# Performance work log

Measured on AMD Instinct MI355X. Metric: run time of the kernel, lower is better.

Reference implementation:

```python
import jax, jax.numpy as jnp
import numpy as np
import math

B, C, H, W = 8, 64, 256, 256
E, NH = 256, 8
HD = E // NH  # 32


def get_coords(h, w):
    xx, yy = jnp.meshgrid(jnp.arange(h, dtype=jnp.float32), jnp.arange(w, dtype=jnp.float32), indexing='ij')
    return jnp.stack((xx.reshape(-1), yy.reshape(-1)), axis=-1)  # [N, 2]


def setup_inputs() -> dict:
    key = jax.random.key(0)
    ks = jax.random.split(key, 12)
    def xavier(k, shape):
        fan_out, fan_in = shape
        a = math.sqrt(6.0 / (fan_in + fan_out))
        return jax.random.uniform(k, shape, jnp.float32, -a, a)
    x = jax.random.normal(ks[0], (B, C, H, W), jnp.float32)
    z = jax.random.normal(ks[1], (B, C), jnp.float32)
    pos = jax.random.uniform(ks[2], (B, NH, 2), jnp.float32) * (H - 1)
    Wq = xavier(ks[3], (E, C)); bq = jnp.zeros((E,), jnp.float32)
    Wk = xavier(ks[4], (E, C)); bk = jnp.zeros((E,), jnp.float32)
    Wv = xavier(ks[5], (E, C)); bv = jnp.zeros((E,), jnp.float32)
    Wp = xavier(ks[6], (HD, 2)); bp = jax.random.uniform(ks[7], (HD,), jnp.float32, -1.0, 1.0) / math.sqrt(2.0)
    return {"x": x, "z": z, "pos": pos, "Wq": Wq, "bq": bq, "Wk": Wk, "bk": bk,
            "Wv": Wv, "bv": bv, "Wp": Wp, "bp": bp}


def reference(x, z, pos, Wq, bq, Wk, bk, Wv, bv, Wp, bp):
    b, c, h, w = x.shape
    n = h * w
    x_flat = x.reshape(b, c, n).transpose(0, 2, 1)          # [B, N, C]
    pos_grid = get_coords(h, w)                              # [N, 2]
    q = (z @ Wq.T + bq).reshape(b, NH, HD)                   # [B, H, hd]
    k = (x_flat @ Wk.T + bk).reshape(b, n, NH, HD)           # [B, N, H, hd]
    # relative-position modulation of keys
    rel = pos_grid[None, :, None, :] - pos[:, None, :, :]    # [B, N, H, 2]
    qxk = rel @ Wp.T + bp                                    # [B, N, H, hd]
    k = k * qxk
    v = x_flat @ Wv.T + bv                                   # [B, N, E]
    attn_logits = jnp.einsum('bhc,bnhc->bnh', q, k) / math.sqrt(HD)
    attention = jax.nn.softmax(attn_logits, axis=1)          # softmax over N
    pos_out = jnp.einsum('bnh,nx->bhx', attention, pos_grid) # [B, H, 2]
    values = jnp.einsum('bnh,bnc->bhc', attention, v)        # [B, H, E]
    return (values, pos_out)
```

## Files before the change

### kernel.cpp

```cpp
#include <hip/hip_runtime.h>

#define NN    65536
#define NSUB  256
#define NBLK  (NN/NSUB)

typedef short bf16x8 __attribute__((ext_vector_type(8)));
typedef float f32x4v __attribute__((ext_vector_type(4)));
typedef unsigned short ushort_t;
typedef unsigned int uint_t;

#define XSTR   72
#define XHI_B  0
#define XLO_B  36864
#define LGA_B  36864
#define LGSTR  28
#define RED_B  73728
#define SMEM_BYTES 74240

#define WTHI_B  0
#define WTLO_B  32768
#define CJ_B    65536
#define PM_B    66304
#define PL_B    131840
#define PSP_B   197376
#define PSX_B   328448
#define Q_B     4522752
#define QSTR    68

__device__ __forceinline__ uint_t bf16_rne_bits(float f) {
  uint_t u = __float_as_uint(f);
  return (u + 0x7FFFu + ((u >> 16) & 1u)) >> 16;
}
template <int CTRL>
__device__ __forceinline__ float dpp_add(float x) {
  int t = __builtin_amdgcn_update_dpp(0, __float_as_int(x), CTRL, 0xf, 0xf, false);
  return x + __int_as_float(t);
}
template <int CTRL>
__device__ __forceinline__ float dpp_maxs(float x) {
  int t = __builtin_amdgcn_update_dpp((int)0xFF800000u, __float_as_int(x), CTRL, 0xf, 0xf, false);
  return fmaxf(x, __int_as_float(t));
}
__device__ __forceinline__ float wave_sum(float x) {
  x = dpp_add<0x111>(x); x = dpp_add<0x112>(x); x = dpp_add<0x114>(x);
  x = dpp_add<0x118>(x); x = dpp_add<0x142>(x); x = dpp_add<0x143>(x);
  return __int_as_float(__builtin_amdgcn_readlane(__float_as_int(x), 63));
}
__device__ __forceinline__ float wave_max(float x) {
  x = dpp_maxs<0x111>(x); x = dpp_maxs<0x112>(x); x = dpp_maxs<0x114>(x);
  x = dpp_maxs<0x118>(x); x = dpp_maxs<0x142>(x); x = dpp_maxs<0x143>(x);
  return __int_as_float(__builtin_amdgcn_readlane(__float_as_int(x), 63));
}

__global__ __launch_bounds__(64) void prep_kernel(
    const float* __restrict__ z,  const float* __restrict__ Wq, const float* __restrict__ bq,
    const float* __restrict__ Wk, const float* __restrict__ bk,
    const float* __restrict__ Wp, const float* __restrict__ bp,
    ushort_t* __restrict__ WThi, ushort_t* __restrict__ WTlo, float* __restrict__ Cj)
{
  const int h = blockIdx.x, b = blockIdx.y, t = threadIdx.x;
  __shared__ float q[32];
  if (t < 32) {
    const int e = h*32 + t;
    float a = bq[e];
    const float* zr = z + b*64;
    const float* wr = Wq + e*64;
    #pragma unroll 8
    for (int c = 0; c < 64; ++c) a += zr[c]*wr[c];
    q[t] = a;
  }
  __syncthreads();
  const int c = t;
  float w[3] = {0.f, 0.f, 0.f};
  #pragma unroll 4
  for (int hd = 0; hd < 32; ++hd) {
    const float qk = q[hd] * Wk[(h*32+hd)*64 + c];
    w[0] += qk * bp[hd];
    w[1] += qk * Wp[hd*2+0];
    w[2] += qk * Wp[hd*2+1];
  }
  #pragma unroll
  for (int j = 0; j < 3; ++j) {
    const int coeff = h*3 + j;
    const uint_t hb = bf16_rne_bits(w[j]);
    const float  fh = __uint_as_float(hb << 16);
    const uint_t lb = bf16_rne_bits(w[j] - fh);
    WThi[(b*32 + coeff)*64 + c] = (ushort_t)hb;
    WTlo[(b*32 + coeff)*64 + c] = (ushort_t)lb;
  }
  if (h == 0) {
    #pragma unroll
    for (int r = 0; r < 8; ++r) {
      WThi[(b*32 + 24 + r)*64 + c] = 0;
      WTlo[(b*32 + 24 + r)*64 + c] = 0;
    }
  }
  if (t < 3) {
    float s = 0.f;
    for (int hd = 0; hd < 32; ++hd) {
      const float m = (t == 0) ? bp[hd] : Wp[hd*2 + (t-1)];
      s += q[hd] * m * bk[h*32+hd];
    }
    Cj[b*24 + h*3 + t] = s;
  }
}

__global__ __launch_bounds__(256, 2) void main_kernel(
    const float* __restrict__ x, const float* __restrict__ pos,
    const ushort_t* __restrict__ WThi, const ushort_t* __restrict__ WTlo,
    const float* __restrict__ Cj,
    float* __restrict__ Pm, float* __restrict__ Pl,
    float* __restrict__ Psp, float* __restrict__ Psx)
{
  extern __shared__ char smc[];
  ushort_t* xhi = (ushort_t*)(smc + XHI_B);
  ushort_t* xlo = (ushort_t*)(smc + XLO_B);
  float*    lga = (float*)(smc + LGA_B);
  float*    red = (float*)(smc + RED_B);
  const int t   = threadIdx.x;
  const int blk = blockIdx.x;
  const int b   = blockIdx.y;
  const int n0  = blk * NSUB;
  const int wid = t >> 6, lid = t & 63;
  const int c0  = lid & 15, q4 = lid >> 4;

  bf16x8 bh[2][2], bl[2][2];
  {
    const ushort_t* wtb_h = WThi + b*2048;
    const ushort_t* wtb_l = WTlo + b*2048;
    #pragma unroll
    for (int nt = 0; nt < 2; ++nt)
      #pragma unroll
      for (int ks = 0; ks < 2; ++ks) {
        const int off = (nt*16 + c0)*64 + ks*32 + q4*8;
        bh[nt][ks] = *(const bf16x8*)(wtb_h + off);
        bl[nt][ks] = *(const bf16x8*)(wtb_l + off);
      }
  }

  {
    const float* xg = x + (size_t)b*64*NN + n0 + t;
    #pragma unroll
    for (int cc = 0; cc < 4; ++cc) {
      float v[16];
      #pragma unroll
      for (int i = 0; i < 16; ++i) v[i] = xg[(size_t)(cc*16+i)*NN];
      uint_t hb[16], lb[16];
      #pragma unroll
      for (int i = 0; i < 16; ++i) {
        hb[i] = bf16_rne_bits(v[i]);
        lb[i] = bf16_rne_bits(v[i] - __uint_as_float(hb[i] << 16));
      }
      uint4 H0 = make_uint4(hb[0]|(hb[1]<<16), hb[2]|(hb[3]<<16), hb[4]|(hb[5]<<16), hb[6]|(hb[7]<<16));
      uint4 H1 = make_uint4(hb[8]|(hb[9]<<16), hb[10]|(hb[11]<<16), hb[12]|(hb[13]<<16), hb[14]|(hb[15]<<16));
      uint4 L0 = make_uint4(lb[0]|(lb[1]<<16), lb[2]|(lb[3]<<16), lb[4]|(lb[5]<<16), lb[6]|(lb[7]<<16));
      uint4 L1 = make_uint4(lb[8]|(lb[9]<<16), lb[10]|(lb[11]<<16), lb[12]|(lb[13]<<16), lb[14]|(lb[15]<<16));
      char* dh = smc + XHI_B + t*144 + cc*32;
      char* dl = smc + XLO_B + t*144 + cc*32;
      *(uint4*)(dh)      = H0;  *(uint4*)(dh + 16) = H1;
      *(uint4*)(dl)      = L0;  *(uint4*)(dl + 16) = L1;
    }
  }

  float cj[24];
  {
    const float* cjp = Cj + b*24;
    #pragma unroll
    for (int k = 0; k < 24; ++k) cj[k] = cjp[k];
  }
  float rxh[8], py[8];
  #pragma unroll
  for (int h = 0; h < 8; ++h) {
    rxh[h] = (float)blk - pos[(b*8+h)*2 + 0];
    py[h]  = pos[(b*8+h)*2 + 1];
  }

  __syncthreads();

  f32x4v acc[4][2];
  #pragma unroll
  for (int mt = 0; mt < 4; ++mt) { acc[mt][0] = (f32x4v)0.f; acc[mt][1] = (f32x4v)0.f; }
  {
    const int mrow0 = wid*64;
    #pragma unroll
    for (int mt = 0; mt < 4; ++mt) {
      const int row = mrow0 + mt*16 + c0;
      const ushort_t* ph = xhi + row*XSTR + q4*8;
      const ushort_t* pl = xlo + row*XSTR + q4*8;
      bf16x8 ah0 = *(const bf16x8*)(ph);
      bf16x8 ah1 = *(const bf16x8*)(ph + 32);
      bf16x8 al0 = *(const bf16x8*)(pl);
      bf16x8 al1 = *(const bf16x8*)(pl + 32);
      #pragma unroll
      for (int nt = 0; nt < 2; ++nt) {
        f32x4v a = acc[mt][nt];
        a = __builtin_amdgcn_mfma_f32_16x16x32_bf16(ah0, bh[nt][0], a, 0, 0, 0);
        a = __builtin_amdgcn_mfma_f32_16x16x32_bf16(ah1, bh[nt][1], a, 0, 0, 0);
        a = __builtin_amdgcn_mfma_f32_16x16x32_bf16(ah0, bl[nt][0], a, 0, 0, 0);
        a = __builtin_amdgcn_mfma_f32_16x16x32_bf16(ah1, bl[nt][1], a, 0, 0, 0);
        a = __builtin_amdgcn_mfma_f32_16x16x32_bf16(al0, bh[nt][0], a, 0, 0, 0);
        a = __builtin_amdgcn_mfma_f32_16x16x32_bf16(al1, bh[nt][1], a, 0, 0, 0);
        acc[mt][nt] = a;
      }
    }
  }
  __syncthreads();

  {
    const int mrow0 = wid*64;
    #pragma unroll
    for (int mt = 0; mt < 4; ++mt)
      #pragma unroll
      for (int r = 0; r < 4; ++r) {
        const int prow = mrow0 + mt*16 + q4*4 + r;
        lga[prow*LGSTR + c0] = acc[mt][0][r];
        if (c0 < 8) lga[prow*LGSTR + 16 + c0] = acc[mt][1][r];
      }
  }
  __syncthreads();

  float a24[24];
  {
    const float4* ap = (const float4*)(lga + t*LGSTR);
    #pragma unroll
    for (int r = 0; r < 6; ++r) *(float4*)(a24 + 4*r) = ap[r];
  }
  const float tf = (float)t;
  float lg[8];
  #pragma unroll
  for (int h = 0; h < 8; ++h) {
    const float a0 = a24[h*3+0] + cj[h*3+0];
    const float a1 = a24[h*3+1] + cj[h*3+1];
    const float a2 = a24[h*3+2] + cj[h*3+2];
    lg[h] = (a0 + rxh[h]*a1 + (tf - py[h])*a2) * 0.17677669529663687f;
  }

  #pragma unroll
  for (int h = 0; h < 8; ++h) {
    const float m = wave_max(lg[h]);
    if (lid == 0) red[h*4 + wid] = m;
  }
  __syncthreads();

  float p[8];
  #pragma unroll
  for (int h = 0; h < 8; ++h) {
    const float M = fmaxf(fmaxf(red[h*4+0], red[h*4+1]), fmaxf(red[h*4+2], red[h*4+3]));
    p[h] = __expf(lg[h] - M);
  }
  #pragma unroll
  for (int h = 0; h < 8; ++h) {
    const float sp  = wave_sum(p[h]);
    const float spj = wave_sum(p[h] * tf);
    if (lid == 0) { red[32 + h*4 + wid] = sp; red[64 + h*4 + wid] = spj; }
  }
  __syncthreads();

  if (t < 8) {
    const int base = (b*NBLK + blk)*8 + t;
    const float M = fmaxf(fmaxf(red[t*4+0], red[t*4+1]), fmaxf(red[t*4+2], red[t*4+3]));
    const float L  = red[32+t*4+0] + red[32+t*4+1] + red[32+t*4+2] + red[32+t*4+3];
    const float SJ = red[64+t*4+0] + red[64+t*4+1] + red[64+t*4+2] + red[64+t*4+3];
    Pm[base] = M;
    Pl[base] = L;
    Psp[base*2+0] = (float)blk * L;
    Psp[base*2+1] = SJ;
  }

  float aB[8];
  #pragma unroll
  for (int h = 0; h < 8; ++h) aB[h] = 0.f;
  {
    const ushort_t* xrow = xhi + (wid*64)*XSTR + lid;
    #pragma unroll 8
    for (int j = 0; j < 64; ++j) {
      const float xv = __uint_as_float(((uint_t)xrow[j*XSTR]) << 16);
      #pragma unroll
      for (int h = 0; h < 8; ++h) {
        const float pj = __int_as_float(__builtin_amdgcn_readlane(__float_as_int(p[h]), j));
        aB[h] = fmaf(pj, xv, aB[h]);
      }
    }
  }
  __syncthreads();
  {
    float* pstage = (float*)smc;
    #pragma unroll
    for (int h = 0; h < 8; ++h) pstage[(wid*8 + h)*64 + lid] = aB[h];
  }
  __syncthreads();
  {
    const float* pstage = (const float*)smc;
    const size_t pb = ((size_t)(b*NBLK + blk))*8;
    #pragma unroll
    for (int r = 0; r < 2; ++r) {
      const int idx = t + 256*r;
      const float s = pstage[idx] + pstage[512+idx] + pstage[1024+idx] + pstage[1536+idx];
      Psx[pb*64 + idx] = s;
    }
  }
}

__global__ __launch_bounds__(256) void reduce1_kernel(
    const float* __restrict__ Pm, const float* __restrict__ Pl,
    const float* __restrict__ Psp, const float* __restrict__ Psx,
    float* __restrict__ Q)
{
  const int g = blockIdx.x, h = blockIdx.y, b = blockIdx.z, t = threadIdx.x;
  __shared__ float al[32];
  __shared__ float mgs;
  __shared__ float sums[3];
  __shared__ float sxl[256];
  const int base = (b*NBLK + g*32)*8 + h;

  float m_t = -1e30f;
  if (t < 32) m_t = Pm[base + t*8];
  if (t < 64) {
    float mm = m_t;
    #pragma unroll
    for (int off = 16; off >= 1; off >>= 1) mm = fmaxf(mm, __shfl_xor(mm, off, 64));
    if (t == 0) mgs = mm;
  }
  __syncthreads();
  const float Mg = mgs;
  if (t < 32) {
    const float a = __expf(m_t - Mg);
    al[t] = a;
    float lt = Pl[base + t*8] * a;
    float sx = Psp[(base + t*8)*2 + 0] * a;
    float sy = Psp[(base + t*8)*2 + 1] * a;
    #pragma unroll
    for (int off = 16; off >= 1; off >>= 1) {
      lt += __shfl_xor(lt, off, 64);
      sx += __shfl_xor(sx, off, 64);
      sy += __shfl_xor(sy, off, 64);
    }
    if (t == 0) { sums[0] = lt; sums[1] = sx; sums[2] = sy; }
  }
  __syncthreads();
  {
    const int c = t & 63, g2 = t >> 6;
    float acc = 0.f;
    #pragma unroll
    for (int i = 0; i < 8; ++i) {
      const int k = g2*8 + i;
      acc += al[k] * Psx[(size_t)(base + k*8)*64 + c];
    }
    sxl[g2*64 + c] = acc;
  }
  __syncthreads();
  float* q = Q + ((b*8 + h)*8 + g)*QSTR;
  if (t < 64) q[4+t] = sxl[t] + sxl[64+t] + sxl[128+t] + sxl[192+t];
  if (t == 0) { q[0] = Mg; q[1] = sums[0]; q[2] = sums[1]; q[3] = sums[2]; }
}

__global__ __launch_bounds__(64) void reduce2_kernel(
    const float* __restrict__ Q, const float* __restrict__ Wv, const float* __restrict__ bv,
    float* __restrict__ out)
{
  const int h = blockIdx.x, b = blockIdx.y, t = threadIdx.x;
  __shared__ float qm[8], bl[8], l8[8], sx8[8], sy8[8];
  __shared__ float SXs[64];
  const float* qb = Q + ((b*8 + h)*8)*QSTR;

  if (t < 8) qm[t] = qb[t*QSTR + 0];
  __syncthreads();
  float M = qm[0];
  #pragma unroll
  for (int g = 1; g < 8; ++g) M = fmaxf(M, qm[g]);
  if (t < 8) {
    const float be = __expf(qm[t] - M);
    bl[t]  = be;
    l8[t]  = be * qb[t*QSTR + 1];
    sx8[t] = be * qb[t*QSTR + 2];
    sy8[t] = be * qb[t*QSTR + 3];
  }
  __syncthreads();
  float L = 0.f;
  #pragma unroll
  for (int g = 0; g < 8; ++g) L += l8[g];
  const float invL = 1.0f / L;
  {
    float s = 0.f;
    #pragma unroll
    for (int g = 0; g < 8; ++g) s += bl[g] * qb[g*QSTR + 4 + t];
    SXs[t] = s * invL;
  }
  __syncthreads();

  #pragma unroll
  for (int r = 0; r < 4; ++r) {
    const int e = t + 64*r;
    float v = bv[e];
    const float* wvr = Wv + e*64;
    #pragma unroll 8
    for (int c = 0; c < 64; ++c) v += wvr[c] * SXs[c];
    out[(b*8 + h)*256 + e] = v;
  }
  if (t == 0) {
    float spx = 0.f, spy = 0.f;
    #pragma unroll
    for (int g = 0; g < 8; ++g) { spx += sx8[g]; spy += sy8[g]; }
    out[16384 + (b*8 + h)*2 + 0] = spx * invL;
    out[16384 + (b*8 + h)*2 + 1] = spy * invL;
  }
}

extern "C" void kernel_launch(void* const* d_in, const int* in_sizes, int n_in,
                              void* d_out, int out_size, void* d_ws, size_t ws_size,
                              hipStream_t stream)
{
  const float* x   = (const float*)d_in[0];
  const float* z   = (const float*)d_in[1];
  const float* pos = (const float*)d_in[2];
  const float* Wq  = (const float*)d_in[3];
  const float* bq  = (const float*)d_in[4];
  const float* Wk  = (const float*)d_in[5];
  const float* bk  = (const float*)d_in[6];
  const float* Wv  = (const float*)d_in[7];
  const float* bv  = (const float*)d_in[8];
  const float* Wp  = (const float*)d_in[9];
  const float* bp  = (const float*)d_in[10];
  float* out = (float*)d_out;
  char*  wsb = (char*)d_ws;

  ushort_t* WThi = (ushort_t*)(wsb + WTHI_B);
  ushort_t* WTlo = (ushort_t*)(wsb + WTLO_B);
  float* Cj  = (float*)(wsb + CJ_B);
  float* Pm  = (float*)(wsb + PM_B);
  float* Pl  = (float*)(wsb + PL_B);
  float* Psp = (float*)(wsb + PSP_B);
  float* Psx = (float*)(wsb + PSX_B);
  float* Q   = (float*)(wsb + Q_B);

  (void)hipFuncSetAttribute((const void*)main_kernel,
                            hipFuncAttributeMaxDynamicSharedMemorySize, SMEM_BYTES);

  prep_kernel   <<<dim3(8,8),    64,  0,          stream>>>(z, Wq, bq, Wk, bk, Wp, bp, WThi, WTlo, Cj);
  main_kernel   <<<dim3(NBLK,8), 256, SMEM_BYTES, stream>>>(x, pos, WThi, WTlo, Cj, Pm, Pl, Psp, Psx);
  reduce1_kernel<<<dim3(8,8,8),  256, 0,          stream>>>(Pm, Pl, Psp, Psx, Q);
  reduce2_kernel<<<dim3(8,8),    64,  0,          stream>>>(Q, Wv, bv, out);
}
```

Before: 248.0 us.

## Process two row tiles per block with online softmax and register prefetch

Each main-kernel block now handles two 256-pixel tiles in sequence. It keeps running max, sum and position statistics with online-softmax rescaling, and prefetches the second tile's 64 channels into registers while the first tile is processed. This halves the grid and the partial-result traffic into the reduction kernels, and packed bf16 conversion is used where available. The cost is 64 extra live registers per thread under launch_bounds(256,2), which risks spills or lower occupancy, plus fewer blocks to hide memory latency.

```diff
diff --git a/kernel.cpp b/kernel.cpp
--- a/kernel.cpp
+++ b/kernel.cpp
@@ -1,8 +1,7 @@
 #include <hip/hip_runtime.h>
 
-#define NN    65536
-#define NSUB  256
-#define NBLK  (NN/NSUB)
+#define NN     65536
+#define NBLK2  128
 
 typedef short bf16x8 __attribute__((ext_vector_type(8)));
 typedef float f32x4v __attribute__((ext_vector_type(4)));
@@ -21,15 +20,28 @@
 #define WTLO_B  32768
 #define CJ_B    65536
 #define PM_B    66304
-#define PL_B    131840
-#define PSP_B   197376
-#define PSX_B   328448
-#define Q_B     4522752
+#define PL_B    99072
+#define PSP_B   131840
+#define PSX_B   197376
+#define Q_B     2294528
 #define QSTR    68
 
 __device__ __forceinline__ uint_t bf16_rne_bits(float f) {
   uint_t u = __float_as_uint(f);
   return (u + 0x7FFFu + ((u >> 16) & 1u)) >> 16;
+}
+__device__ __forceinline__ uint_t pack2_bf16(float f0, float f1) {
+#if __has_builtin(__builtin_amdgcn_cvt_pk_bf16_f32)
+  auto r = __builtin_amdgcn_cvt_pk_bf16_f32(f0, f1);
+  if constexpr (sizeof(r) == 4) {
+    uint_t u; __builtin_memcpy(&u, &r, 4);
+    return u;
+  } else {
+    return bf16_rne_bits(f0) | (bf16_rne_bits(f1) << 16);
+  }
+#else
+  return bf16_rne_bits(f0) | (bf16_rne_bits(f1) << 16);
+#endif
 }
 template <int CTRL>
 __device__ __forceinline__ float dpp_add(float x) {
@@ -120,9 +132,13 @@
   const int t   = threadIdx.x;
   const int blk = blockIdx.x;
   const int b   = blockIdx.y;
-  const int n0  = blk * NSUB;
   const int wid = t >> 6, lid = t & 63;
   const int c0  = lid & 15, q4 = lid >> 4;
+
+  float F[64];
+  const float* xg = x + (size_t)b*64*NN + (size_t)blk*512 + t;
+  #pragma unroll
+  for (int c = 0; c < 64; ++c) F[c] = xg[(size_t)c*NN];
 
   bf16x8 bh[2][2], bl[2][2];
   {
@@ -137,151 +153,175 @@
         bl[nt][ks] = *(const bf16x8*)(wtb_l + off);
       }
   }
-
-  {
-    const float* xg = x + (size_t)b*64*NN + n0 + t;
+  float cj[24];
+  {
+    const float* cjp = Cj + b*24;
+    #pragma unroll
+    for (int k = 0; k < 24; ++k) cj[k] = cjp[k];
+  }
+  float posx[8], py[8];
+  #pragma unroll
+  for (int h = 0; h < 8; ++h) {
+    posx[h] = pos[(b*8+h)*2 + 0];
+    py[h]   = pos[(b*8+h)*2 + 1];
+  }
+
+  float Mrun[8], Lrun[8], SJrun[8], SPXrun[8], aB[8];
+  #pragma unroll
+  for (int h = 0; h < 8; ++h) {
+    Mrun[h] = -1e30f; Lrun[h] = 0.f; SJrun[h] = 0.f; SPXrun[h] = 0.f; aB[h] = 0.f;
+  }
+
+  const float tf = (float)t;
+
+  #pragma unroll 1
+  for (int tile = 0; tile < 2; ++tile) {
+    __syncthreads();
+
     #pragma unroll
     for (int cc = 0; cc < 4; ++cc) {
-      float v[16];
-      #pragma unroll
-      for (int i = 0; i < 16; ++i) v[i] = xg[(size_t)(cc*16+i)*NN];
-      uint_t hb[16], lb[16];
-      #pragma unroll
-      for (int i = 0; i < 16; ++i) {
-        hb[i] = bf16_rne_bits(v[i]);
-        lb[i] = bf16_rne_bits(v[i] - __uint_as_float(hb[i] << 16));
+      uint_t H[8], L[8];
+      #pragma unroll
+      for (int i = 0; i < 8; ++i) {
+        const float f0 = F[cc*16 + 2*i], f1 = F[cc*16 + 2*i + 1];
+        const uint_t hp = pack2_bf16(f0, f1);
+        const float r0 = f0 - __uint_as_float(hp << 16);
+        const float r1 = f1 - __uint_as_float(hp & 0xFFFF0000u);
+        H[i] = hp;
+        L[i] = pack2_bf16(r0, r1);
       }
-      uint4 H0 = make_uint4(hb[0]|(hb[1]<<16), hb[2]|(hb[3]<<16), hb[4]|(hb[5]<<16), hb[6]|(hb[7]<<16));
-      uint4 H1 = make_uint4(hb[8]|(hb[9]<<16), hb[10]|(hb[11]<<16), hb[12]|(hb[13]<<16), hb[14]|(hb[15]<<16));
-      uint4 L0 = make_uint4(lb[0]|(lb[1]<<16), lb[2]|(lb[3]<<16), lb[4]|(lb[5]<<16), lb[6]|(lb[7]<<16));
-      uint4 L1 = make_uint4(lb[8]|(lb[9]<<16), lb[10]|(lb[11]<<16), lb[12]|(lb[13]<<16), lb[14]|(lb[15]<<16));
       char* dh = smc + XHI_B + t*144 + cc*32;
       char* dl = smc + XLO_B + t*144 + cc*32;
-      *(uint4*)(dh)      = H0;  *(uint4*)(dh + 16) = H1;
-      *(uint4*)(dl)      = L0;  *(uint4*)(dl + 16) = L1;
-    }
-  }
-
-  float cj[24];
-  {
-    const float* cjp = Cj + b*24;
-    #pragma unroll
-    for (int k = 0; k < 24; ++k) cj[k] = cjp[k];
-  }
-  float rxh[8], py[8];
-  #pragma unroll
-  for (int h = 0; h < 8; ++h) {
-    rxh[h] = (float)blk - pos[(b*8+h)*2 + 0];
-    py[h]  = pos[(b*8+h)*2 + 1];
-  }
-
-  __syncthreads();
-
-  f32x4v acc[4][2];
-  #pragma unroll
-  for (int mt = 0; mt < 4; ++mt) { acc[mt][0] = (f32x4v)0.f; acc[mt][1] = (f32x4v)0.f; }
-  {
-    const int mrow0 = wid*64;
-    #pragma unroll
-    for (int mt = 0; mt < 4; ++mt) {
-      const int row = mrow0 + mt*16 + c0;
-      const ushort_t* ph = xhi + row*XSTR + q4*8;
-      const ushort_t* pl = xlo + row*XSTR + q4*8;
-      bf16x8 ah0 = *(const bf16x8*)(ph);
-      bf16x8 ah1 = *(const bf16x8*)(ph + 32);
-      bf16x8 al0 = *(const bf16x8*)(pl);
-      bf16x8 al1 = *(const bf16x8*)(pl + 32);
-      #pragma unroll
-      for (int nt = 0; nt < 2; ++nt) {
-        f32x4v a = acc[mt][nt];
-        a = __builtin_amdgcn_mfma_f32_16x16x32_bf16(ah0, bh[nt][0], a, 0, 0, 0);
-        a = __builtin_amdgcn_mfma_f32_16x16x32_bf16(ah1, bh[nt][1], a, 0, 0, 0);
-        a = __builtin_amdgcn_mfma_f32_16x16x32_bf16(ah0, bl[nt][0], a, 0, 0, 0);
-        a = __builtin_amdgcn_mfma_f32_16x16x32_bf16(ah1, bl[nt][1], a, 0, 0, 0);
-        a = __builtin_amdgcn_mfma_f32_16x16x32_bf16(al0, bh[nt][0], a, 0, 0, 0);
-        a = __builtin_amdgcn_mfma_f32_16x16x32_bf16(al1, bh[nt][1], a, 0, 0, 0);
-        acc[mt][nt] = a;
+      *(uint4*)(dh)      = make_uint4(H[0],H[1],H[2],H[3]);
+      *(uint4*)(dh + 16) = make_uint4(H[4],H[5],H[6],H[7]);
+      *(uint4*)(dl)      = make_uint4(L[0],L[1],L[2],L[3]);
+      *(uint4*)(dl + 16) = make_uint4(L[4],L[5],L[6],L[7]);
+    }
+    __syncthreads();
+
+    f32x4v acc[4][2];
+    #pragma unroll
+    for (int mt = 0; mt < 4; ++mt) { acc[mt][0] = (f32x4v)0.f; acc[mt][1] = (f32x4v)0.f; }
+    {
+      const int mrow0 = wid*64;
+      #pragma unroll
+      for (int mt = 0; mt < 4; ++mt) {
+        const int row = mrow0 + mt*16 + c0;
+        const ushort_t* ph = xhi + row*XSTR + q4*8;
+        const ushort_t* pl = xlo + row*XSTR + q4*8;
+        bf16x8 ah0 = *(const bf16x8*)(ph);
+        bf16x8 ah1 = *(const bf16x8*)(ph + 32);
+        bf16x8 al0 = *(const bf16x8*)(pl);
+        bf16x8 al1 = *(const bf16x8*)(pl + 32);
+        #pragma unroll
+        for (int nt = 0; nt < 2; ++nt) {
+          f32x4v a = acc[mt][nt];
+          a = __builtin_amdgcn_mfma_f32_16x16x32_bf16(ah0, bh[nt][0], a, 0, 0, 0);
+          a = __builtin_amdgcn_mfma_f32_16x16x32_bf16(ah1, bh[nt][1], a, 0, 0, 0);
+          a = __builtin_amdgcn_mfma_f32_16x16x32_bf16(ah0, bl[nt][0], a, 0, 0, 0);
+          a = __builtin_amdgcn_mfma_f32_16x16x32_bf16(ah1, bl[nt][1], a, 0, 0, 0);
+          a = __builtin_amdgcn_mfma_f32_16x16x32_bf16(al0, bh[nt][0], a, 0, 0, 0);
+          a = __builtin_amdgcn_mfma_f32_16x16x32_bf16(al1, bh[nt][1], a, 0, 0, 0);
+          acc[mt][nt] = a;
+        }
       }
     }
-  }
-  __syncthreads();
-
-  {
-    const int mrow0 = wid*64;
-    #pragma unroll
-    for (int mt = 0; mt < 4; ++mt)
-      #pragma unroll
-      for (int r = 0; r < 4; ++r) {
-        const int prow = mrow0 + mt*16 + q4*4 + r;
-        lga[prow*LGSTR + c0] = acc[mt][0][r];
-        if (c0 < 8) lga[prow*LGSTR + 16 + c0] = acc[mt][1][r];
+    __syncthreads();
+
+    {
+      const int mrow0 = wid*64;
+      #pragma unroll
+      for (int mt = 0; mt < 4; ++mt)
+        #pragma unroll
+        for (int r = 0; r < 4; ++r) {
+          const int prow = mrow0 + mt*16 + q4*4 + r;
+          lga[prow*LGSTR + c0] = acc[mt][0][r];
+          if (c0 < 8) lga[prow*LGSTR + 16 + c0] = acc[mt][1][r];
+        }
+    }
+    __syncthreads();
+
+    float a24[24];
+    {
+      const float4* ap = (const float4*)(lga + t*LGSTR);
+      #pragma unroll
+      for (int r = 0; r < 6; ++r) *(float4*)(a24 + 4*r) = ap[r];
+    }
+    const float gxf = (float)(2*blk + tile);
+    float lg[8];
+    #pragma unroll
+    for (int h = 0; h < 8; ++h) {
+      const float a0 = a24[h*3+0] + cj[h*3+0];
+      const float a1 = a24[h*3+1] + cj[h*3+1];
+      const float a2 = a24[h*3+2] + cj[h*3+2];
+      lg[h] = (a0 + (gxf - posx[h])*a1 + (tf - py[h])*a2) * 0.17677669529663687f;
+    }
+
+    #pragma unroll
+    for (int h = 0; h < 8; ++h) {
+      const float m = wave_max(lg[h]);
+      if (lid == 0) red[h*4 + wid] = m;
+    }
+    __syncthreads();
+
+    float p[8], alpha[8];
+    #pragma unroll
+    for (int h = 0; h < 8; ++h) {
+      const float Mt = fmaxf(fmaxf(red[h*4+0], red[h*4+1]), fmaxf(red[h*4+2], red[h*4+3]));
+      const float Mn = fmaxf(Mrun[h], Mt);
+      alpha[h] = __expf(Mrun[h] - Mn);
+      Mrun[h]  = Mn;
+      p[h]     = __expf(lg[h] - Mn);
+      aB[h]   *= alpha[h];
+    }
+    #pragma unroll
+    for (int h = 0; h < 8; ++h) {
+      const float sp  = wave_sum(p[h]);
+      const float spj = wave_sum(p[h] * tf);
+      if (lid == 0) { red[32 + h*4 + wid] = sp; red[64 + h*4 + wid] = spj; }
+    }
+    __syncthreads();
+
+    #pragma unroll
+    for (int h = 0; h < 8; ++h) {
+      const float Lt  = red[32+h*4+0] + red[32+h*4+1] + red[32+h*4+2] + red[32+h*4+3];
+      const float SJt = red[64+h*4+0] + red[64+h*4+1] + red[64+h*4+2] + red[64+h*4+3];
+      Lrun[h]   = Lrun[h]*alpha[h]   + Lt;
+      SJrun[h]  = SJrun[h]*alpha[h]  + SJt;
+      SPXrun[h] = SPXrun[h]*alpha[h] + gxf*Lt;
+    }
+
+    if (tile == 0) {
+      const float* xg1 = xg + 256;
+      #pragma unroll
+      for (int c = 0; c < 64; ++c) F[c] = xg1[(size_t)c*NN];
+    }
+
+    {
+      const ushort_t* xrow = xhi + (wid*64)*XSTR + lid;
+      #pragma unroll 8
+      for (int j = 0; j < 64; ++j) {
+        const float xv = __uint_as_float(((uint_t)xrow[j*XSTR]) << 16);
+        #pragma unroll
+        for (int h = 0; h < 8; ++h) {
+          const float pj = __int_as_float(__builtin_amdgcn_readlane(__float_as_int(p[h]), j));
+          aB[h] = fmaf(pj, xv, aB[h]);
+        }
       }
-  }
-  __syncthreads();
-
-  float a24[24];
-  {
-    const float4* ap = (const float4*)(lga + t*LGSTR);
-    #pragma unroll
-    for (int r = 0; r < 6; ++r) *(float4*)(a24 + 4*r) = ap[r];
-  }
-  const float tf = (float)t;
-  float lg[8];
-  #pragma unroll
-  for (int h = 0; h < 8; ++h) {
-    const float a0 = a24[h*3+0] + cj[h*3+0];
-    const float a1 = a24[h*3+1] + cj[h*3+1];
-    const float a2 = a24[h*3+2] + cj[h*3+2];
-    lg[h] = (a0 + rxh[h]*a1 + (tf - py[h])*a2) * 0.17677669529663687f;
-  }
-
-  #pragma unroll
-  for (int h = 0; h < 8; ++h) {
-    const float m = wave_max(lg[h]);
-    if (lid == 0) red[h*4 + wid] = m;
-  }
-  __syncthreads();
-
-  float p[8];
-  #pragma unroll
-  for (int h = 0; h < 8; ++h) {
-    const float M = fmaxf(fmaxf(red[h*4+0], red[h*4+1]), fmaxf(red[h*4+2], red[h*4+3]));
-    p[h] = __expf(lg[h] - M);
-  }
-  #pragma unroll
-  for (int h = 0; h < 8; ++h) {
-    const float sp  = wave_sum(p[h]);
-    const float spj = wave_sum(p[h] * tf);
-    if (lid == 0) { red[32 + h*4 + wid] = sp; red[64 + h*4 + wid] = spj; }
-  }
-  __syncthreads();
-
-  if (t < 8) {
-    const int base = (b*NBLK + blk)*8 + t;
-    const float M = fmaxf(fmaxf(red[t*4+0], red[t*4+1]), fmaxf(red[t*4+2], red[t*4+3]));
-    const float L  = red[32+t*4+0] + red[32+t*4+1] + red[32+t*4+2] + red[32+t*4+3];
-    const float SJ = red[64+t*4+0] + red[64+t*4+1] + red[64+t*4+2] + red[64+t*4+3];
-    Pm[base] = M;
-    Pl[base] = L;
-    Psp[base*2+0] = (float)blk * L;
-    Psp[base*2+1] = SJ;
-  }
-
-  float aB[8];
-  #pragma unroll
-  for (int h = 0; h < 8; ++h) aB[h] = 0.f;
-  {
-    const ushort_t* xrow = xhi + (wid*64)*XSTR + lid;
-    #pragma unroll 8
-    for (int j = 0; j < 64; ++j) {
-      const float xv = __uint_as_float(((uint_t)xrow[j*XSTR]) << 16);
-      #pragma unroll
-      for (int h = 0; h < 8; ++h) {
-        const float pj = __int_as_float(__builtin_amdgcn_readlane(__float_as_int(p[h]), j));
-        aB[h] = fmaf(pj, xv, aB[h]);
-      }
-    }
-  }
+    }
+  }
+
+  const int base = (b*NBLK2 + blk)*8;
+  if (t == 0) {
+    #pragma unroll
+    for (int h = 0; h < 8; ++h) {
+      Pm[base + h] = Mrun[h];
+      Pl[base + h] = Lrun[h];
+      Psp[(base + h)*2 + 0] = SPXrun[h];
+      Psp[(base + h)*2 + 1] = SJrun[h];
+    }
+  }
+
   __syncthreads();
   {
     float* pstage = (float*)smc;
@@ -291,12 +331,11 @@
   __syncthreads();
   {
     const float* pstage = (const float*)smc;
-    const size_t pb = ((size_t)(b*NBLK + blk))*8;
     #pragma unroll
     for (int r = 0; r < 2; ++r) {
       const int idx = t + 256*r;
       const float s = pstage[idx] + pstage[512+idx] + pstage[1024+idx] + pstage[1536+idx];
-      Psx[pb*64 + idx] = s;
+      Psx[(size_t)base*64 + idx] = s;
     }
   }
 }
@@ -311,7 +350,7 @@
   __shared__ float mgs;
   __shared__ float sums[3];
   __shared__ float sxl[256];
-  const int base = (b*NBLK + g*32)*8 + h;
+  const int base = (b*NBLK2 + g*32)*8 + h;
 
   float m_t = -1e30f;
   if (t < 32) m_t = Pm[base + t*8];
@@ -349,7 +388,7 @@
     sxl[g2*64 + c] = acc;
   }
   __syncthreads();
-  float* q = Q + ((b*8 + h)*8 + g)*QSTR;
+  float* q = Q + ((b*8 + h)*4 + g)*QSTR;
   if (t < 64) q[4+t] = sxl[t] + sxl[64+t] + sxl[128+t] + sxl[192+t];
   if (t == 0) { q[0] = Mg; q[1] = sums[0]; q[2] = sums[1]; q[3] = sums[2]; }
 }
@@ -359,31 +398,27 @@
     float* __restrict__ out)
 {
   const int h = blockIdx.x, b = blockIdx.y, t = threadIdx.x;
-  __shared__ float qm[8], bl[8], l8[8], sx8[8], sy8[8];
+  __shared__ float qm[4], bl[4], l4[4], sx4[4], sy4[4];
   __shared__ float SXs[64];
-  const float* qb = Q + ((b*8 + h)*8)*QSTR;
-
-  if (t < 8) qm[t] = qb[t*QSTR + 0];
-  __syncthreads();
-  float M = qm[0];
-  #pragma unroll
-  for (int g = 1; g < 8; ++g) M = fmaxf(M, qm[g]);
-  if (t < 8) {
+  const float* qb = Q + ((b*8 + h)*4)*QSTR;
+
+  if (t < 4) qm[t] = qb[t*QSTR + 0];
+  __syncthreads();
+  float M = fmaxf(fmaxf(qm[0], qm[1]), fmaxf(qm[2], qm[3]));
+  if (t < 4) {
     const float be = __expf(qm[t] - M);
     bl[t]  = be;
-    l8[t]  = be * qb[t*QSTR + 1];
-    sx8[t] = be * qb[t*QSTR + 2];
-    sy8[t] = be * qb[t*QSTR + 3];
-  }
-  __syncthreads();
-  float L = 0.f;
-  #pragma unroll
-  for (int g = 0; g < 8; ++g) L += l8[g];
+    l4[t]  = be * qb[t*QSTR + 1];
+    sx4[t] = be * qb[t*QSTR + 2];
+    sy4[t] = be * qb[t*QSTR + 3];
+  }
+  __syncthreads();
+  const float L = l4[0] + l4[1] + l4[2] + l4[3];
   const float invL = 1.0f / L;
   {
     float s = 0.f;
     #pragma unroll
-    for (int g = 0; g < 8; ++g) s += bl[g] * qb[g*QSTR + 4 + t];
+    for (int g = 0; g < 4; ++g) s += bl[g] * qb[g*QSTR + 4 + t];
     SXs[t] = s * invL;
   }
   __syncthreads();
@@ -398,11 +433,10 @@
     out[(b*8 + h)*256 + e] = v;
   }
   if (t == 0) {
-    float spx = 0.f, spy = 0.f;
-    #pragma unroll
-    for (int g = 0; g < 8; ++g) { spx += sx8[g]; spy += sy8[g]; }
-    out[16384 + (b*8 + h)*2 + 0] = spx * invL;
-    out[16384 + (b*8 + h)*2 + 1] = spy * invL;
+    const float SPx = sx4[0] + sx4[1] + sx4[2] + sx4[3];
+    const float SPy = sy4[0] + sy4[1] + sy4[2] + sy4[3];
+    out[16384 + (b*8 + h)*2 + 0] = SPx * invL;
+    out[16384 + (b*8 + h)*2 + 1] = SPy * invL;
   }
 }
 
@@ -436,8 +470,8 @@
   (void)hipFuncSetAttribute((const void*)main_kernel,
                             hipFuncAttributeMaxDynamicSharedMemorySize, SMEM_BYTES);
 
-  prep_kernel   <<<dim3(8,8),    64,  0,          stream>>>(z, Wq, bq, Wk, bk, Wp, bp, WThi, WTlo, Cj);
-  main_kernel   <<<dim3(NBLK,8), 256, SMEM_BYTES, stream>>>(x, pos, WThi, WTlo, Cj, Pm, Pl, Psp, Psx);
-  reduce1_kernel<<<dim3(8,8,8),  256, 0,          stream>>>(Pm, Pl, Psp, Psx, Q);
-  reduce2_kernel<<<dim3(8,8),    64,  0,          stream>>>(Q, Wv, bv, out);
-}
+  prep_kernel   <<<dim3(8,8),     64,  0,          stream>>>(z, Wq, bq, Wk, bk, Wp, bp, WThi, WTlo, Cj);
+  main_kernel   <<<dim3(NBLK2,8), 256, SMEM_BYTES, stream>>>(x, pos, WThi, WTlo, Cj, Pm, Pl, Psp, Psx);
+  reduce1_kernel<<<dim3(4,8,8),   256, 0,          stream>>>(Pm, Pl, Psp, Psx, Q);
+  reduce2_kernel<<<dim3(8,8),     64,  0,          stream>>>(Q, Wv, bv, out);
+}
```

New measurement: 344.9 us. 39.0% more time.
